# Kernel tuning notes

Hardware: AMD Instinct MI355X
Metric: run time of the kernel (lower is better)

Reference implementation:

```python
import jax, jax.numpy as jnp
import numpy as np

T, M, D_IN, N = 4096, 512, 11, 51


def setup_inputs() -> dict:
    key = jax.random.key(0)
    ks = jax.random.split(key, 11)
    s = 1.0 / np.sqrt(N)  # torch LSTMCell/Linear default init scale
    return {
        "input": jax.random.normal(ks[0], (T, M, D_IN), dtype=jnp.float32),
        "W_ih1": jax.random.uniform(ks[1], (4 * N, D_IN), jnp.float32, -s, s),
        "W_hh1": jax.random.uniform(ks[2], (4 * N, N), jnp.float32, -s, s),
        "b_ih1": jax.random.uniform(ks[3], (4 * N,), jnp.float32, -s, s),
        "b_hh1": jax.random.uniform(ks[4], (4 * N,), jnp.float32, -s, s),
        "W_ih2": jax.random.uniform(ks[5], (4 * N, N), jnp.float32, -s, s),
        "W_hh2": jax.random.uniform(ks[6], (4 * N, N), jnp.float32, -s, s),
        "b_ih2": jax.random.uniform(ks[7], (4 * N,), jnp.float32, -s, s),
        "b_hh2": jax.random.uniform(ks[8], (4 * N,), jnp.float32, -s, s),
        "W_lin": jax.random.uniform(ks[9], (1, N), jnp.float32, -s, s),
        "b_lin": jax.random.uniform(ks[10], (1,), jnp.float32, -s, s),
        "future": 0,
    }


def _lstm_cell(x, h, c, W_ih, W_hh, b_ih, b_hh):
    # torch gate order: input, forget, cell(g), output
    gates = x @ W_ih.T + b_ih + h @ W_hh.T + b_hh  # [m, 4n]
    i, f, g, o = jnp.split(gates, 4, axis=-1)
    c_new = jax.nn.sigmoid(f) * c + jax.nn.sigmoid(i) * jnp.tanh(g)
    h_new = jax.nn.sigmoid(o) * jnp.tanh(c_new)
    return h_new, c_new


def reference(input, W_ih1, W_hh1, b_ih1, b_hh1, W_ih2, W_hh2, b_ih2, b_hh2,
              W_lin, b_lin, future):
    m = input.shape[1]
    n = W_hh1.shape[1]
    h1 = jnp.zeros((m, n), jnp.float32)
    c1 = jnp.zeros((m, n), jnp.float32)
    h2 = jnp.zeros((m, n), jnp.float32)
    c2 = jnp.zeros((m, n), jnp.float32)

    def step(carry, x_t):
        h1, c1, h2, c2 = carry
        h1, c1 = _lstm_cell(x_t, h1, c1, W_ih1, W_hh1, b_ih1, b_hh1)
        h2, c2 = _lstm_cell(h1, h2, c2, W_ih2, W_hh2, b_ih2, b_hh2)
        out = h2 @ W_lin.T + b_lin  # [m, 1]
        return (h1, c1, h2, c2), out

    _, outs = jax.lax.scan(step, (h1, c1, h2, c2), input)  # [T, m, 1]
    # torch.stack(outputs, 1).squeeze(2) -> [m, T]
    # (future loop is dimensionally invalid in the original for future>0; future=0)
    return outs[:, :, 0].T
```

## Files before the change

### kernel.cpp

```cpp
#include <hip/hip_runtime.h>

#define T_STEPS 4096
#define M_BATCH 512
#define D_INP   11
#define N_HID   51

typedef float v4f __attribute__((ext_vector_type(4)));

__device__ __forceinline__ float sigmoid_fast(float v) {
    return __builtin_amdgcn_rcpf(1.0f + __expf(-v));
}
__device__ __forceinline__ float tanh_fast(float v) {
    return 2.0f * __builtin_amdgcn_rcpf(1.0f + __expf(-2.0f * v)) - 1.0f;
}
__device__ __forceinline__ float RL(float v, int l) {
    return __uint_as_float(__builtin_amdgcn_readlane(__float_as_uint(v), l));
}

__attribute__((amdgpu_waves_per_eu(2, 2)))
__global__ __launch_bounds__(256)
void lstm2_sgprbc(const float* __restrict__ input,
                  const float* __restrict__ W_ih1, const float* __restrict__ W_hh1,
                  const float* __restrict__ b_ih1, const float* __restrict__ b_hh1,
                  const float* __restrict__ W_ih2, const float* __restrict__ W_hh2,
                  const float* __restrict__ b_ih2, const float* __restrict__ b_hh2,
                  const float* __restrict__ W_lin, const float* __restrict__ b_lin,
                  float* __restrict__ out)
{
    const int  tid   = threadIdx.x;
    const int  col   = blockIdx.x;
    const int  wid   = tid >> 6;
    const int  lane  = tid & 63;
    const bool valid = lane < N_HID;
    const int  ln    = valid ? lane : 0;

    __shared__ __align__(16) float hstate[2][112];
    __shared__ __align__(16) float xs[2][64 * 12];
    __shared__ __align__(16) v4f   pl1[64];
    __shared__ __align__(16) v4f   pl2[3][64];
    __shared__ float outbuf[128];

    v4f wA[31], wB[10];
    v4f biasv = {0.f, 0.f, 0.f, 0.f};
    float wlin = 0.f;
    const float blin = b_lin[0];
    float cstate = 0.f;

    if (wid == 0) {
        #pragma unroll
        for (int q = 0; q < 4; ++q) {
            const int r = q * N_HID + ln;
            biasv[q] = valid ? (b_ih1[r] + b_hh1[r]) : 0.f;
            #pragma unroll
            for (int i = 0; i < 11; ++i) wA[i][q] = W_ih1[r * D_INP + i];
            #pragma unroll
            for (int i = 11; i < 31; ++i) wA[i][q] = W_hh1[r * N_HID + (i - 11)];
            #pragma unroll
            for (int j = 0; j < 10; ++j) wB[j][q] = W_ih2[r * N_HID + j];
        }
    } else if (wid == 1) {
        #pragma unroll
        for (int q = 0; q < 4; ++q) {
            const int r = q * N_HID + ln;
            #pragma unroll
            for (int i = 0; i < 31; ++i) wA[i][q] = W_hh1[r * N_HID + 20 + i];
            #pragma unroll
            for (int j = 0; j < 10; ++j) wB[j][q] = W_ih2[r * N_HID + 10 + j];
        }
    } else if (wid == 2) {
        #pragma unroll
        for (int q = 0; q < 4; ++q) {
            const int r = q * N_HID + ln;
            biasv[q] = valid ? (b_ih2[r] + b_hh2[r]) : 0.f;
            #pragma unroll
            for (int i = 0; i < 31; ++i) wA[i][q] = W_ih2[r * N_HID + 20 + i];
            #pragma unroll
            for (int j = 0; j < 10; ++j) wB[j][q] = W_hh2[r * N_HID + j];
        }
        wlin = valid ? W_lin[ln] : 0.f;
    } else {
        #pragma unroll
        for (int q = 0; q < 4; ++q) {
            const int r = q * N_HID + ln;
            #pragma unroll
            for (int i = 0; i < 31; ++i) wA[i][q] = W_hh2[r * N_HID + 10 + i];
            #pragma unroll
            for (int j = 0; j < 10; ++j) wB[j][q] = W_hh2[r * N_HID + 41 + j];
        }
    }

    auto xload = [&](int c, int e) -> float {
        int s = e / 11, d = e - s * 11;
        int tc = c * 64 + s; if (tc > T_STEPS - 1) tc = T_STEPS - 1;
        return input[((size_t)tc * M_BATCH + col) * D_INP + d];
    };
    auto xput = [&](int buf, int e, float v) {
        int s = e / 11, d = e - s * 11;
        xs[buf][s * 12 + d] = v;
    };

    for (int i = tid; i < 2 * 112; i += 256) (&hstate[0][0])[i] = 0.f;
    for (int i = tid; i < 2 * 64 * 12; i += 256) (&xs[0][0])[i] = 0.f;
    for (int i = tid; i < 64; i += 256) { pl1[i] = (v4f){0,0,0,0};
        pl2[0][i] = (v4f){0,0,0,0}; pl2[1][i] = (v4f){0,0,0,0}; pl2[2][i] = (v4f){0,0,0,0}; }
    __syncthreads();
    {
        xput(0, tid, xload(0, tid));
        xput(0, tid + 256, xload(0, tid + 256));
        if (tid < 192) xput(0, tid + 512, xload(0, tid + 512));
    }
    __syncthreads();

    float xr0 = 0.f, xr1 = 0.f, xr2 = 0.f;

    #pragma unroll 1
    for (int t = 0; t <= T_STEPS; ++t) {
        if ((t & 63) == 0) {
            const int c = (t >> 6) + 1;
            xr0 = xload(c, tid);
            xr1 = xload(c, tid + 256);
            if (tid < 192) xr2 = xload(c, tid + 512);
        }

        const float* hs = &hstate[t & 1][0];
        v4f accA = {0.f,0.f,0.f,0.f}, accB = {0.f,0.f,0.f,0.f};
        float actv;

        if (wid == 0) {
            const float* xp = &xs[(t >> 6) & 1][(t & 63) * 12];
            actv = (lane < D_INP) ? xp[lane]
                                  : hs[(lane - D_INP) < N_HID - 1 ? (lane - D_INP) : N_HID - 1];
            #pragma unroll
            for (int i = 0; i < 31; ++i) {
                const float a = RL(actv, i);
                accA += wA[i] * a;
                if (i >= 11 && i < 21) accB += wB[i - 11] * a;
            }
        } else if (wid == 1) {
            actv = hs[10 + (lane < 41 ? lane : 40)];
            #pragma unroll
            for (int j = 0; j < 10; ++j) accB += wB[j] * RL(actv, j);
            #pragma unroll
            for (int i = 0; i < 31; ++i) accA += wA[i] * RL(actv, 10 + i);
        } else if (wid == 2) {
            actv = (lane < 31) ? hs[20 + lane]
                               : hs[56 + ((lane - 31) < 10 ? (lane - 31) : 9)];
            #pragma unroll
            for (int i = 0; i < 31; ++i) accA += wA[i] * RL(actv, i);
            #pragma unroll
            for (int j = 0; j < 10; ++j) accA += wB[j] * RL(actv, 31 + j);
        } else {
            actv = hs[56 + 10 + (lane < 41 ? lane : 40)];
            #pragma unroll
            for (int i = 0; i < 31; ++i) accA += wA[i] * RL(actv, i);
            #pragma unroll
            for (int j = 0; j < 10; ++j) accA += wB[j] * RL(actv, 31 + j);
        }

        if (valid) {
            if (wid == 0)      pl2[0][lane] = accB;
            else if (wid == 1) { pl1[lane] = accA; pl2[1][lane] = accB; }
            else if (wid == 3) pl2[2][lane] = accA;
        }
        __syncthreads();

        if (wid == 0) {
            const v4f g = accA + pl1[lane] + biasv;
            const float si = sigmoid_fast(g.x), sf = sigmoid_fast(g.y);
            const float tg = tanh_fast(g.z),    so = sigmoid_fast(g.w);
            cstate = sf * cstate + si * tg;
            const float hv = so * tanh_fast(cstate);
            if (valid) hstate[(t + 1) & 1][lane] = hv;
        } else if (wid == 2) {
            if (t >= 1) {
                const v4f g = accA + pl2[0][lane] + pl2[1][lane] + pl2[2][lane] + biasv;
                const float si = sigmoid_fast(g.x), sf = sigmoid_fast(g.y);
                const float tg = tanh_fast(g.z),    so = sigmoid_fast(g.w);
                cstate = sf * cstate + si * tg;
                const float hv = so * tanh_fast(cstate);
                if (valid) hstate[(t + 1) & 1][56 + lane] = hv;
                float part = valid ? wlin * hv : 0.f;
                #pragma unroll
                for (int off = 32; off > 0; off >>= 1)
                    part += __shfl_down(part, off, 64);
                if (lane == 0) outbuf[(t - 1) & 127] = part + blin;
            }
        } else if (wid == 1) {
            if ((t & 63) == 1 && t >= 65) {
                const int tb = (t - 65) + lane;
                out[(size_t)col * T_STEPS + tb] = outbuf[tb & 127];
            }
        }

        if ((t & 63) == 32) {
            const int buf = ((t >> 6) + 1) & 1;
            xput(buf, tid, xr0);
            xput(buf, tid + 256, xr1);
            if (tid < 192) xput(buf, tid + 512, xr2);
        }
        __syncthreads();
    }

    if (wid == 1) {
        const int idx = 4032 + lane;
        out[(size_t)col * T_STEPS + idx] = outbuf[idx & 127];
    }
}

extern "C" void kernel_launch(void* const* d_in, const int* in_sizes, int n_in,
                              void* d_out, int out_size, void* d_ws, size_t ws_size,
                              hipStream_t stream) {
    const float* input = (const float*)d_in[0];
    const float* W_ih1 = (const float*)d_in[1];
    const float* W_hh1 = (const float*)d_in[2];
    const float* b_ih1 = (const float*)d_in[3];
    const float* b_hh1 = (const float*)d_in[4];
    const float* W_ih2 = (const float*)d_in[5];
    const float* W_hh2 = (const float*)d_in[6];
    const float* b_ih2 = (const float*)d_in[7];
    const float* b_hh2 = (const float*)d_in[8];
    const float* W_lin = (const float*)d_in[9];
    const float* b_lin = (const float*)d_in[10];
    float* out = (float*)d_out;

    lstm2_sgprbc<<<M_BATCH, 256, 0, stream>>>(
        input, W_ih1, W_hh1, b_ih1, b_hh1,
        W_ih2, W_hh2, b_ih2, b_hh2, W_lin, b_lin, out);
}
```

Before: 5.275 ms.

## Replicate LSTM cell updates across waves to keep hidden state in registers

Instead of one wave computing each layer's cell update and publishing h through a shared hidden-state buffer, waves 0-2 each redundantly compute layer-1 cell updates and waves 2-3 compute layer-2 updates. Each wave then keeps its own copy of h1/h2 in registers and broadcasts it with readlane, which drops the shared-memory h write and read from the per-step critical path. The weight partition is reshuffled to match, and the x row for the next step is preloaded into a register. The cost is redundant transcendental work in several waves and more partial-sum buffers in LDS.

```diff
diff --git a/kernel.cpp b/kernel.cpp
--- a/kernel.cpp
+++ b/kernel.cpp
@@ -19,75 +19,58 @@
 
 __attribute__((amdgpu_waves_per_eu(2, 2)))
 __global__ __launch_bounds__(256)
-void lstm2_sgprbc(const float* __restrict__ input,
-                  const float* __restrict__ W_ih1, const float* __restrict__ W_hh1,
-                  const float* __restrict__ b_ih1, const float* __restrict__ b_hh1,
-                  const float* __restrict__ W_ih2, const float* __restrict__ W_hh2,
-                  const float* __restrict__ b_ih2, const float* __restrict__ b_hh2,
-                  const float* __restrict__ W_lin, const float* __restrict__ b_lin,
-                  float* __restrict__ out)
+void lstm2_replk(const float* __restrict__ input,
+                 const float* __restrict__ W_ih1, const float* __restrict__ W_hh1,
+                 const float* __restrict__ b_ih1, const float* __restrict__ b_hh1,
+                 const float* __restrict__ W_ih2, const float* __restrict__ W_hh2,
+                 const float* __restrict__ b_ih2, const float* __restrict__ b_hh2,
+                 const float* __restrict__ W_lin, const float* __restrict__ b_lin,
+                 float* __restrict__ out)
 {
     const int  tid   = threadIdx.x;
     const int  col   = blockIdx.x;
     const int  wid   = tid >> 6;
     const int  lane  = tid & 63;
     const bool valid = lane < N_HID;
-    const int  ln    = valid ? lane : 0;
+    const int  ln    = valid ? lane : N_HID - 1;
 
-    __shared__ __align__(16) float hstate[2][112];
+    __shared__ __align__(16) v4f   pl1[2][64];
+    __shared__ __align__(16) v4f   pl2[3][64];
     __shared__ __align__(16) float xs[2][64 * 12];
-    __shared__ __align__(16) v4f   pl1[64];
-    __shared__ __align__(16) v4f   pl2[3][64];
     __shared__ float outbuf[128];
 
-    v4f wA[31], wB[10];
-    v4f biasv = {0.f, 0.f, 0.f, 0.f};
+    v4f wv[41];
+    v4f b1v = {0.f,0.f,0.f,0.f}, b2v = {0.f,0.f,0.f,0.f};
     float wlin = 0.f;
     const float blin = b_lin[0];
-    float cstate = 0.f;
+    float c1 = 0.f, h1r = 0.f, c2 = 0.f, h2r = 0.f;
 
-    if (wid == 0) {
-        #pragma unroll
-        for (int q = 0; q < 4; ++q) {
-            const int r = q * N_HID + ln;
-            biasv[q] = valid ? (b_ih1[r] + b_hh1[r]) : 0.f;
+    #pragma unroll
+    for (int q = 0; q < 4; ++q) {
+        const int r = q * N_HID + ln;
+        if (wid <= 2) b1v[q] = b_ih1[r] + b_hh1[r];
+        if (wid >= 2) b2v[q] = b_ih2[r] + b_hh2[r];
+        if (wid == 0) {
             #pragma unroll
-            for (int i = 0; i < 11; ++i) wA[i][q] = W_ih1[r * D_INP + i];
+            for (int i = 0; i < 11; ++i) wv[i][q]      = W_ih1[r * D_INP + i];
             #pragma unroll
-            for (int i = 11; i < 31; ++i) wA[i][q] = W_hh1[r * N_HID + (i - 11)];
+            for (int i = 0; i < 30; ++i) wv[11 + i][q] = W_hh1[r * N_HID + i];
+        } else if (wid == 1) {
             #pragma unroll
-            for (int j = 0; j < 10; ++j) wB[j][q] = W_ih2[r * N_HID + j];
-        }
-    } else if (wid == 1) {
-        #pragma unroll
-        for (int q = 0; q < 4; ++q) {
-            const int r = q * N_HID + ln;
+            for (int i = 0; i < 21; ++i) wv[i][q]      = W_hh1[r * N_HID + 30 + i];
             #pragma unroll
-            for (int i = 0; i < 31; ++i) wA[i][q] = W_hh1[r * N_HID + 20 + i];
+            for (int j = 0; j < 20; ++j) wv[21 + j][q] = W_ih2[r * N_HID + j];
+        } else if (wid == 2) {
             #pragma unroll
-            for (int j = 0; j < 10; ++j) wB[j][q] = W_ih2[r * N_HID + 10 + j];
-        }
-    } else if (wid == 2) {
-        #pragma unroll
-        for (int q = 0; q < 4; ++q) {
-            const int r = q * N_HID + ln;
-            biasv[q] = valid ? (b_ih2[r] + b_hh2[r]) : 0.f;
+            for (int i = 0; i < 31; ++i) wv[i][q]      = W_ih2[r * N_HID + 20 + i];
             #pragma unroll
-            for (int i = 0; i < 31; ++i) wA[i][q] = W_ih2[r * N_HID + 20 + i];
+            for (int j = 0; j < 10; ++j) wv[31 + j][q] = W_hh2[r * N_HID + j];
+        } else {
             #pragma unroll
-            for (int j = 0; j < 10; ++j) wB[j][q] = W_hh2[r * N_HID + j];
-        }
-        wlin = valid ? W_lin[ln] : 0.f;
-    } else {
-        #pragma unroll
-        for (int q = 0; q < 4; ++q) {
-            const int r = q * N_HID + ln;
-            #pragma unroll
-            for (int i = 0; i < 31; ++i) wA[i][q] = W_hh2[r * N_HID + 10 + i];
-            #pragma unroll
-            for (int j = 0; j < 10; ++j) wB[j][q] = W_hh2[r * N_HID + 41 + j];
+            for (int i = 0; i < 41; ++i) wv[i][q]      = W_hh2[r * N_HID + 10 + i];
         }
     }
+    if (wid == 3) wlin = valid ? W_lin[lane] : 0.f;
 
     auto xload = [&](int c, int e) -> float {
         int s = e / 11, d = e - s * 11;
@@ -99,10 +82,7 @@
         xs[buf][s * 12 + d] = v;
     };
 
-    for (int i = tid; i < 2 * 112; i += 256) (&hstate[0][0])[i] = 0.f;
-    for (int i = tid; i < 2 * 64 * 12; i += 256) (&xs[0][0])[i] = 0.f;
-    for (int i = tid; i < 64; i += 256) { pl1[i] = (v4f){0,0,0,0};
-        pl2[0][i] = (v4f){0,0,0,0}; pl2[1][i] = (v4f){0,0,0,0}; pl2[2][i] = (v4f){0,0,0,0}; }
+    for (int i = tid; i < 2 * 768; i += 256) (&xs[0][0])[i] = 0.f;
     __syncthreads();
     {
         xput(0, tid, xload(0, tid));
@@ -111,6 +91,8 @@
     }
     __syncthreads();
 
+    const int xln = (lane < D_INP) ? lane : (D_INP - 1);
+    float xv = (wid == 0) ? xs[0][xln] : 0.f;
     float xr0 = 0.f, xr1 = 0.f, xr2 = 0.f;
 
     #pragma unroll 1
@@ -122,81 +104,67 @@
             if (tid < 192) xr2 = xload(c, tid + 512);
         }
 
-        const float* hs = &hstate[t & 1][0];
-        v4f accA = {0.f,0.f,0.f,0.f}, accB = {0.f,0.f,0.f,0.f};
-        float actv;
-
+        v4f aP = {0.f,0.f,0.f,0.f}, aS = {0.f,0.f,0.f,0.f};
         if (wid == 0) {
-            const float* xp = &xs[(t >> 6) & 1][(t & 63) * 12];
-            actv = (lane < D_INP) ? xp[lane]
-                                  : hs[(lane - D_INP) < N_HID - 1 ? (lane - D_INP) : N_HID - 1];
             #pragma unroll
-            for (int i = 0; i < 31; ++i) {
-                const float a = RL(actv, i);
-                accA += wA[i] * a;
-                if (i >= 11 && i < 21) accB += wB[i - 11] * a;
-            }
+            for (int k = 0; k < 11; ++k) aP += wv[k] * RL(xv, k);
+            #pragma unroll
+            for (int i = 0; i < 30; ++i) aP += wv[11 + i] * RL(h1r, i);
         } else if (wid == 1) {
-            actv = hs[10 + (lane < 41 ? lane : 40)];
             #pragma unroll
-            for (int j = 0; j < 10; ++j) accB += wB[j] * RL(actv, j);
+            for (int i = 0; i < 21; ++i) aP += wv[i] * RL(h1r, 30 + i);
             #pragma unroll
-            for (int i = 0; i < 31; ++i) accA += wA[i] * RL(actv, 10 + i);
+            for (int j = 0; j < 20; ++j) aS += wv[21 + j] * RL(h1r, j);
         } else if (wid == 2) {
-            actv = (lane < 31) ? hs[20 + lane]
-                               : hs[56 + ((lane - 31) < 10 ? (lane - 31) : 9)];
             #pragma unroll
-            for (int i = 0; i < 31; ++i) accA += wA[i] * RL(actv, i);
+            for (int i = 0; i < 31; ++i) aP += wv[i] * RL(h1r, 20 + i);
             #pragma unroll
-            for (int j = 0; j < 10; ++j) accA += wB[j] * RL(actv, 31 + j);
+            for (int j = 0; j < 10; ++j) aP += wv[31 + j] * RL(h2r, j);
         } else {
-            actv = hs[56 + 10 + (lane < 41 ? lane : 40)];
             #pragma unroll
-            for (int i = 0; i < 31; ++i) accA += wA[i] * RL(actv, i);
-            #pragma unroll
-            for (int j = 0; j < 10; ++j) accA += wB[j] * RL(actv, 31 + j);
+            for (int i = 0; i < 41; ++i) aP += wv[i] * RL(h2r, 10 + i);
         }
 
-        if (valid) {
-            if (wid == 0)      pl2[0][lane] = accB;
-            else if (wid == 1) { pl1[lane] = accA; pl2[1][lane] = accB; }
-            else if (wid == 3) pl2[2][lane] = accA;
-        }
+        if (wid == 0)      pl1[0][lane] = aP;
+        else if (wid == 1) { pl1[1][lane] = aP; pl2[0][lane] = aS; }
+        else if (wid == 2) pl2[1][lane] = aP;
+        else               pl2[2][lane] = aP;
         __syncthreads();
 
-        if (wid == 0) {
-            const v4f g = accA + pl1[lane] + biasv;
-            const float si = sigmoid_fast(g.x), sf = sigmoid_fast(g.y);
-            const float tg = tanh_fast(g.z),    so = sigmoid_fast(g.w);
-            cstate = sf * cstate + si * tg;
-            const float hv = so * tanh_fast(cstate);
-            if (valid) hstate[(t + 1) & 1][lane] = hv;
-        } else if (wid == 2) {
-            if (t >= 1) {
-                const v4f g = accA + pl2[0][lane] + pl2[1][lane] + pl2[2][lane] + biasv;
-                const float si = sigmoid_fast(g.x), sf = sigmoid_fast(g.y);
-                const float tg = tanh_fast(g.z),    so = sigmoid_fast(g.w);
-                cstate = sf * cstate + si * tg;
-                const float hv = so * tanh_fast(cstate);
-                if (valid) hstate[(t + 1) & 1][56 + lane] = hv;
-                float part = valid ? wlin * hv : 0.f;
+        if (wid <= 2) {
+            const v4f g1 = pl1[0][lane] + pl1[1][lane] + b1v;
+            const float i1 = sigmoid_fast(g1.x), f1 = sigmoid_fast(g1.y);
+            const float gg = tanh_fast(g1.z),    o1 = sigmoid_fast(g1.w);
+            c1  = f1 * c1 + i1 * gg;
+            h1r = o1 * tanh_fast(c1);
+        }
+        if (wid >= 2 && t >= 1) {
+            const v4f g2 = pl2[0][lane] + pl2[1][lane] + pl2[2][lane] + b2v;
+            const float i2 = sigmoid_fast(g2.x), f2 = sigmoid_fast(g2.y);
+            const float gg = tanh_fast(g2.z),    o2 = sigmoid_fast(g2.w);
+            c2  = f2 * c2 + i2 * gg;
+            h2r = o2 * tanh_fast(c2);
+            if (wid == 3) {
+                float part = wlin * h2r;
                 #pragma unroll
                 for (int off = 32; off > 0; off >>= 1)
                     part += __shfl_down(part, off, 64);
                 if (lane == 0) outbuf[(t - 1) & 127] = part + blin;
             }
-        } else if (wid == 1) {
-            if ((t & 63) == 1 && t >= 65) {
-                const int tb = (t - 65) + lane;
-                out[(size_t)col * T_STEPS + tb] = outbuf[tb & 127];
-            }
         }
-
+        if (wid == 1 && (t & 63) == 1 && t >= 65) {
+            const int tb = (t - 65) + lane;
+            out[(size_t)col * T_STEPS + tb] = outbuf[tb & 127];
+        }
         if ((t & 63) == 32) {
             const int buf = ((t >> 6) + 1) & 1;
             xput(buf, tid, xr0);
             xput(buf, tid + 256, xr1);
             if (tid < 192) xput(buf, tid + 512, xr2);
+        }
+        if (wid == 0) {
+            const int tn = t + 1;
+            xv = xs[(tn >> 6) & 1][(tn & 63) * 12 + xln];
         }
         __syncthreads();
     }
@@ -223,7 +191,7 @@
     const float* b_lin = (const float*)d_in[10];
     float* out = (float*)d_out;
 
-    lstm2_sgprbc<<<M_BATCH, 256, 0, stream>>>(
+    lstm2_replk<<<M_BATCH, 256, 0, stream>>>(
         input, W_ih1, W_hh1, b_ih1, b_hh1,
         W_ih2, W_hh2, b_ih2, b_hh2, W_lin, b_lin, out);
 }
```

New measurement: 5.153 ms. 2.3% less time.
